# Optimization experiments

Measured on AMD Instinct MI355X. Metric: run time of the kernel, lower is better.

Reference implementation:

```python
import jax, jax.numpy as jnp
import numpy as np
import math

B, I, O, C = 8192, 1024, 1024, 6


def setup_inputs() -> dict:
    key = jax.random.key(0)
    k1, k2, k3, k4 = jax.random.split(key, 4)
    inputs = jax.random.normal(k1, (B, I), dtype=jnp.float32)
    phase_radians = jax.random.uniform(k2, (B,), dtype=jnp.float32) * (2.0 * math.pi)
    # xavier-uniform per control point: bound = sqrt(6/(I+O))
    bound = math.sqrt(6.0 / (I + O))
    weight_control_points = jax.random.uniform(k3, (C, O, I), dtype=jnp.float32, minval=-bound, maxval=bound)
    bias_control_points = jnp.zeros((C, O), dtype=jnp.float32) + 0.01 * jax.random.normal(k4, (C, O), dtype=jnp.float32)
    return {"inputs": inputs, "phase_radians": phase_radians,
            "weight_control_points": weight_control_points,
            "bias_control_points": bias_control_points}


def _catmull_rom(phase_radians, num_control_points):
    two_pi = 2.0 * math.pi
    phase = jnp.remainder(phase_radians, two_pi)
    position = phase * (float(num_control_points) / two_pi)
    base = jnp.floor(position)
    base_idx = base.astype(jnp.int32)
    t = position - base
    t2 = t * t
    t3 = t2 * t
    indices = jnp.stack([
        jnp.remainder(base_idx - 1, num_control_points),
        jnp.remainder(base_idx, num_control_points),
        jnp.remainder(base_idx + 1, num_control_points),
        jnp.remainder(base_idx + 2, num_control_points),
    ], axis=1)  # [B, 4]
    weights = jnp.stack([
        -0.5 * t + t2 - 0.5 * t3,
        1.0 - 2.5 * t2 + 1.5 * t3,
        0.5 * t + 2.0 * t2 - 1.5 * t3,
        -0.5 * t2 + 0.5 * t3,
    ], axis=1)  # [B, 4]
    return indices, weights


def reference(inputs, phase_radians, weight_control_points, bias_control_points):
    # Faithful to: out[b] = sum_k w[b,k] * (W[idx[b,k]] @ x[b] + bias[idx[b,k]])
    # Instead of materializing [B,O,I] interpolated weights, compute all C
    # control-point projections once and gather the 4 needed per sample.
    num_cp = weight_control_points.shape[0]
    indices, cr_weights = _catmull_rom(phase_radians.astype(inputs.dtype), num_cp)
    y_all = jnp.einsum('coi,bi->bco', weight_control_points, inputs)  # [B, C, O]
    y_sel = jnp.take_along_axis(y_all, indices[:, :, None], axis=1)  # [B, 4, O]
    b_sel = bias_control_points[indices]                              # [B, 4, O]
    return jnp.einsum('bk,bko->bo', cr_weights, y_sel + b_sel)
```

## Files before the change

kernel.cpp:

```cpp
#include <hip/hip_runtime.h>
#include <hip/hip_bf16.h>
#include <math.h>

#define B_SZ 8192
#define I_SZ 1024
#define O_SZ 1024
#define NCP  6

typedef __attribute__((ext_vector_type(8))) short bf16x8;
typedef __attribute__((ext_vector_type(4))) float f32x4;

__device__ __forceinline__ unsigned short f2bf(float f) {
  union { float f; unsigned int u; } v; v.f = f;
  unsigned int u = v.u;
  u += 0x7FFFu + ((u >> 16) & 1u);
  return (unsigned short)(u >> 16);
}

__device__ __forceinline__ int seg_of(float ph) {
  const float two_pi = 6.2831855f;
  const float scale = (float)(6.0 / 6.283185307179586);
  float pm = fmodf(ph, two_pi);
  int bi = (int)floorf(pm * scale);
  return ((bi % NCP) + NCP) % NCP;
}

__global__ __launch_bounds__(1024) void prep_all(
    const float* __restrict__ x, unsigned short* __restrict__ xb,
    const float* __restrict__ w, unsigned short* __restrict__ wb,
    const float* __restrict__ phase,
    unsigned short* __restrict__ perm,
    int* __restrict__ blkinfo) {
  __shared__ int scanbuf[1024][NCP];
  __shared__ int ownh[1024][NCP];
  __shared__ int cum[NCP + 1];
  int t = (int)threadIdx.x;
  int b = (int)blockIdx.x;

  if (b < 1024) {
    const int n4 = B_SZ * I_SZ / 4;
    int idx = b * 1024 + t;
    for (int i = idx; i < n4; i += 1024 * 1024) {
      float4 v = reinterpret_cast<const float4*>(x)[i];
      ushort4 o;
      o.x = f2bf(v.x); o.y = f2bf(v.y); o.z = f2bf(v.z); o.w = f2bf(v.w);
      reinterpret_cast<ushort4*>(xb)[i] = o;
    }
    return;
  }
  if (b < 2048) {
    const int n4 = NCP * O_SZ * I_SZ / 4;
    int idx = (b - 1024) * 1024 + t;
    for (int i = idx; i < n4; i += 1024 * 1024) {
      float4 v = reinterpret_cast<const float4*>(w)[i];
      ushort4 o;
      o.x = f2bf(v.x); o.y = f2bf(v.y); o.z = f2bf(v.z); o.w = f2bf(v.w);
      reinterpret_cast<ushort4*>(wb)[i] = o;
    }
    return;
  }

  int segs[8];
#pragma unroll
  for (int s = 0; s < NCP; ++s) scanbuf[t][s] = 0;
#pragma unroll
  for (int i = 0; i < 8; ++i) {
    segs[i] = seg_of(phase[t * 8 + i]);
    scanbuf[t][segs[i]]++;
  }
#pragma unroll
  for (int s = 0; s < NCP; ++s) ownh[t][s] = scanbuf[t][s];
  __syncthreads();
  for (int d = 1; d < 1024; d <<= 1) {
    int add[NCP];
    if (t >= d) {
#pragma unroll
      for (int s = 0; s < NCP; ++s) add[s] = scanbuf[t - d][s];
    }
    __syncthreads();
    if (t >= d) {
#pragma unroll
      for (int s = 0; s < NCP; ++s) scanbuf[t][s] += add[s];
    }
    __syncthreads();
  }
  if (t == 0) {
    cum[0] = 0;
    for (int s = 0; s < NCP; ++s) cum[s + 1] = cum[s] + scanbuf[1023][s];
  }
  __syncthreads();
#pragma unroll
  for (int s = 0; s < NCP; ++s)
    ownh[t][s] = cum[s] + scanbuf[t][s] - ownh[t][s];
#pragma unroll
  for (int i = 0; i < 8; ++i) {
    int s = segs[i];
    perm[ownh[t][s]++] = (unsigned short)(t * 8 + i);
  }
  if (t < B_SZ / 256) {
    int start = t * 256, end = start + 255;
    int s0 = 0; while (s0 < NCP - 1 && cum[s0 + 1] <= start) ++s0;
    int s1 = 0; while (s1 < NCP - 1 && cum[s1 + 1] <= end) ++s1;
    int nj = s1 - s0 + 4; if (nj > NCP) nj = NCP;
    blkinfo[2 * t] = (s0 + NCP - 1) % NCP;
    blkinfo[2 * t + 1] = nj;
  }
}

__device__ __forceinline__ void gload_lds16(const void* g, void* l) {
  __builtin_amdgcn_global_load_lds(
      (const __attribute__((address_space(1))) void*)g,
      (__attribute__((address_space(3))) void*)l, 16, 0, 0);
}

#define BM 256
#define BN 128
#define BK 64
#define NBUF 3

__global__ __launch_bounds__(512, 1) void pfl_gemm(
    const unsigned short* __restrict__ xb,
    const unsigned short* __restrict__ wb,
    const float* __restrict__ phase,
    const unsigned short* __restrict__ perm,
    const int* __restrict__ blkinfo,
    const float* __restrict__ bias,
    float* __restrict__ out) {
  __shared__ __align__(16) unsigned short Abuf[NBUF][BM * BK];
  __shared__ __align__(16) unsigned short Bbuf[NBUF][BN * BK];
  __shared__ __align__(16) float c4[NCP][BM];
  __shared__ int pblk[BM];

  const int nbn = O_SZ / BN;
  int bid = (int)blockIdx.x;
  int swz = (bid & 7) * 32 + (bid >> 3);
  int rowblk = swz / nbn;
  int brow = rowblk * BM;
  int bcol = (swz % nbn) * BN;

  int tid = (int)threadIdx.x;
  int lane = tid & 63;
  int wid = tid >> 6;
  int wr = wid >> 1;
  int wc = wid & 1;

  int jlo = blkinfo[2 * rowblk];
  int NTb = blkinfo[2 * rowblk + 1] << 4;

  if (tid < BM) {
    int orow = (int)perm[brow + tid];
    pblk[tid] = orow;
    float ph = phase[orow];
    const float two_pi = 6.2831855f;
    float pm = fmodf(ph, two_pi);
    float pos = pm * (float)(6.0 / 6.283185307179586);
    float base = floorf(pos);
    int bi = (int)base;
    float t = pos - base;
    float t2 = t * t, t3 = t2 * t;
    float w0 = -0.5f * t + t2 - 0.5f * t3;
    float w1 = 1.0f - 2.5f * t2 + 1.5f * t3;
    float w2 = 0.5f * t + 2.0f * t2 - 1.5f * t3;
    float w3 = -0.5f * t2 + 0.5f * t3;
    float cc[NCP] = {0.f, 0.f, 0.f, 0.f, 0.f, 0.f};
    cc[((bi - 1) % NCP + NCP) % NCP] += w0;
    cc[(bi % NCP + NCP) % NCP]       += w1;
    cc[((bi + 1) % NCP + NCP) % NCP] += w2;
    cc[((bi + 2) % NCP + NCP) % NCP] += w3;
    for (int j = 0; j < NCP; ++j) c4[j][tid] = cc[j];
  }

  f32x4 acc[4][4];
  f32x4 part[4][4];
#pragma unroll
  for (int m = 0; m < 4; ++m)
#pragma unroll
    for (int n = 0; n < 4; ++n) {
      acc[m][n] = (f32x4){0.f, 0.f, 0.f, 0.f};
      part[m][n] = (f32x4){0.f, 0.f, 0.f, 0.f};
    }

  int swzcol = ((lane & 7) ^ (lane >> 3)) * 8;
  int r0 = brow + wid * 8 + (lane >> 3);
  const unsigned short* xsP0 = xb + (size_t)perm[r0      ] * I_SZ + swzcol;
  const unsigned short* xsP1 = xb + (size_t)perm[r0 +  64] * I_SZ + swzcol;
  const unsigned short* xsP2 = xb + (size_t)perm[r0 + 128] * I_SZ + swzcol;
  const unsigned short* xsP3 = xb + (size_t)perm[r0 + 192] * I_SZ + swzcol;
  const unsigned short* wsrc =
      wb + (size_t)(bcol + wid * 8 + (lane >> 3)) * I_SZ + swzcol;

  int lbase = (lane & 15) * 128 + (((lane >> 4) ^ (lane & 7)) & 7) * 16;

  auto STAGE = [&](int t, int b) {
    int ks = (t & 15) * 64;
    int cN = jlo + (t >> 4); if (cN >= NCP) cN -= NCP;
    const unsigned short* ws = wsrc + (size_t)cN * O_SZ * I_SZ + ks;
    unsigned short* Ad = &Abuf[b][(wid * 8) * BK];
    unsigned short* Bd = &Bbuf[b][(wid * 8) * BK];
    gload_lds16(xsP0 + ks, Ad);
    gload_lds16(xsP1 + ks, Ad + 64 * BK);
    gload_lds16(xsP2 + ks, Ad + 128 * BK);
    gload_lds16(xsP3 + ks, Ad + 192 * BK);
    gload_lds16(ws, Bd);
    gload_lds16(ws + (size_t)64 * I_SZ, Bd + 64 * BK);
  };

  STAGE(0, 0);
  STAGE(1, 1);
  asm volatile("s_waitcnt vmcnt(6)" ::: "memory");
  __builtin_amdgcn_sched_barrier(0);
  __syncthreads();

  int cur = 0;
  for (int t = 0; t < NTb; ++t) {
    const char* Ab = (const char*)&Abuf[cur][0];
    const char* Bb = (const char*)&Bbuf[cur][0];
    int st = cur + 2; if (st >= NBUF) st -= NBUF;

    bf16x8 af0[4], bf0[4], af1[4], bf1[4];
#pragma unroll
    for (int m = 0; m < 4; ++m)
      af0[m] = *reinterpret_cast<const bf16x8*>(
          Ab + (wr * 64 + m * 16) * 128 + lbase);
#pragma unroll
    for (int n = 0; n < 4; ++n)
      bf0[n] = *reinterpret_cast<const bf16x8*>(
          Bb + (wc * 64 + n * 16) * 128 + lbase);
    if (t + 2 < NTb) STAGE(t + 2, st);
    asm volatile("s_waitcnt lgkmcnt(0)" ::: "memory");
    __builtin_amdgcn_sched_barrier(0);

#pragma unroll
    for (int m = 0; m < 4; ++m)
      af1[m] = *reinterpret_cast<const bf16x8*>(
          Ab + (wr * 64 + m * 16) * 128 + (lbase ^ 64));
#pragma unroll
    for (int n = 0; n < 4; ++n)
      bf1[n] = *reinterpret_cast<const bf16x8*>(
          Bb + (wc * 64 + n * 16) * 128 + (lbase ^ 64));
    __builtin_amdgcn_sched_barrier(0);

    __builtin_amdgcn_s_setprio(1);
#pragma unroll
    for (int m = 0; m < 4; ++m)
#pragma unroll
      for (int n = 0; n < 4; ++n)
        part[m][n] = __builtin_amdgcn_mfma_f32_16x16x32_bf16(
            af0[m], bf0[n], part[m][n], 0, 0, 0);
    __builtin_amdgcn_s_setprio(0);

    asm volatile("s_waitcnt lgkmcnt(0)" ::: "memory");
    __builtin_amdgcn_sched_barrier(0);

    __builtin_amdgcn_s_setprio(1);
#pragma unroll
    for (int m = 0; m < 4; ++m)
#pragma unroll
      for (int n = 0; n < 4; ++n)
        part[m][n] = __builtin_amdgcn_mfma_f32_16x16x32_bf16(
            af1[m], bf1[n], part[m][n], 0, 0, 0);
    __builtin_amdgcn_s_setprio(0);

    if ((t & 15) == 15) {
      int cj = jlo + (t >> 4); if (cj >= NCP) cj -= NCP;
#pragma unroll
      for (int m = 0; m < 4; ++m) {
        f32x4 cv = *reinterpret_cast<const f32x4*>(
            &c4[cj][wr * 64 + m * 16 + (lane >> 4) * 4]);
#pragma unroll
        for (int n = 0; n < 4; ++n) {
          acc[m][n] += cv * part[m][n];
          part[m][n] = (f32x4){0.f, 0.f, 0.f, 0.f};
        }
      }
    }

    if (t + 2 < NTb)
      asm volatile("s_waitcnt vmcnt(6)" ::: "memory");
    else
      asm volatile("s_waitcnt vmcnt(0)" ::: "memory");
    __builtin_amdgcn_sched_barrier(0);
    __builtin_amdgcn_s_barrier();
    ++cur; if (cur == NBUF) cur = 0;
  }

#pragma unroll
  for (int n = 0; n < 4; ++n) {
    int col = bcol + wc * 64 + n * 16 + (lane & 15);
    float b6[NCP];
#pragma unroll
    for (int j = 0; j < NCP; ++j) b6[j] = bias[j * O_SZ + col];
#pragma unroll
    for (int m = 0; m < 4; ++m) {
#pragma unroll
      for (int r = 0; r < 4; ++r) {
        int rloc = wr * 64 + m * 16 + (lane >> 4) * 4 + r;
        float s = 0.f;
#pragma unroll
        for (int j = 0; j < NCP; ++j) s += c4[j][rloc] * b6[j];
        out[(size_t)pblk[rloc] * O_SZ + col] = acc[m][n][r] + s;
      }
    }
  }
}

extern "C" void kernel_launch(void* const* d_in, const int* in_sizes, int n_in,
                              void* d_out, int out_size, void* d_ws, size_t ws_size,
                              hipStream_t stream) {
  (void)in_sizes; (void)n_in; (void)out_size; (void)ws_size;
  const float* x     = (const float*)d_in[0];
  const float* phase = (const float*)d_in[1];
  const float* w     = (const float*)d_in[2];
  const float* bias  = (const float*)d_in[3];
  float* out = (float*)d_out;

  char* ws = (char*)d_ws;
  unsigned short* xb = (unsigned short*)ws;
  unsigned short* wb = (unsigned short*)(ws + (size_t)16 * 1024 * 1024);
  unsigned short* perm = (unsigned short*)(ws + (size_t)28 * 1024 * 1024);
  int* blkinfo = (int*)(ws + (size_t)28 * 1024 * 1024 + 16384);

  prep_all<<<2049, 1024, 0, stream>>>(x, xb, w, wb, phase, perm, blkinfo);

  dim3 grid((B_SZ / BM) * (O_SZ / BN));
  pfl_gemm<<<grid, 512, 0, stream>>>(xb, wb, phase, perm, blkinfo, bias, out);
}
```

Before: 110.8 us.

## Software-pipeline LDS fragment loads across barrier to overlap with MFMA

Restructures the main K loop so the first-half A/B fragments for the next tile are read from LDS right after the barrier, while the second-half MFMAs of the current tile are still pending. The first-half MFMAs now issue while the second-half LDS reads are still in flight (lgkmcnt(8)). The goal is to hide LDS read latency behind matrix work instead of stalling on lgkmcnt(0) before each MFMA block. In exchange it keeps two full fragment sets live in registers and makes the barrier and waitcnt ordering more delicate.

```diff
diff --git a/kernel.cpp b/kernel.cpp
--- a/kernel.cpp
+++ b/kernel.cpp
@@ -211,77 +211,94 @@
   __builtin_amdgcn_sched_barrier(0);
   __syncthreads();
 
+  bf16x8 afA[4], bfA[4], afB[4], bfB[4];
+  {
+    const char* Ab = (const char*)&Abuf[0][0];
+    const char* Bb = (const char*)&Bbuf[0][0];
+#pragma unroll
+    for (int m = 0; m < 4; ++m)
+      afA[m] = *reinterpret_cast<const bf16x8*>(
+          Ab + (wr * 64 + m * 16) * 128 + lbase);
+#pragma unroll
+    for (int n = 0; n < 4; ++n)
+      bfA[n] = *reinterpret_cast<const bf16x8*>(
+          Bb + (wc * 64 + n * 16) * 128 + lbase);
+  }
+
   int cur = 0;
   for (int t = 0; t < NTb; ++t) {
     const char* Ab = (const char*)&Abuf[cur][0];
     const char* Bb = (const char*)&Bbuf[cur][0];
     int st = cur + 2; if (st >= NBUF) st -= NBUF;
-
-    bf16x8 af0[4], bf0[4], af1[4], bf1[4];
+    int nxt = cur + 1; if (nxt >= NBUF) nxt -= NBUF;
+
 #pragma unroll
     for (int m = 0; m < 4; ++m)
-      af0[m] = *reinterpret_cast<const bf16x8*>(
-          Ab + (wr * 64 + m * 16) * 128 + lbase);
+      afB[m] = *reinterpret_cast<const bf16x8*>(
+          Ab + (wr * 64 + m * 16) * 128 + (lbase ^ 64));
 #pragma unroll
     for (int n = 0; n < 4; ++n)
-      bf0[n] = *reinterpret_cast<const bf16x8*>(
-          Bb + (wc * 64 + n * 16) * 128 + lbase);
+      bfB[n] = *reinterpret_cast<const bf16x8*>(
+          Bb + (wc * 64 + n * 16) * 128 + (lbase ^ 64));
     if (t + 2 < NTb) STAGE(t + 2, st);
+    asm volatile("s_waitcnt lgkmcnt(8)" ::: "memory");
+    __builtin_amdgcn_sched_barrier(0);
+
+    __builtin_amdgcn_s_setprio(1);
+#pragma unroll
+    for (int m = 0; m < 4; ++m)
+#pragma unroll
+      for (int n = 0; n < 4; ++n)
+        part[m][n] = __builtin_amdgcn_mfma_f32_16x16x32_bf16(
+            afA[m], bfA[n], part[m][n], 0, 0, 0);
+    __builtin_amdgcn_s_setprio(0);
+
     asm volatile("s_waitcnt lgkmcnt(0)" ::: "memory");
     __builtin_amdgcn_sched_barrier(0);
-
-#pragma unroll
-    for (int m = 0; m < 4; ++m)
-      af1[m] = *reinterpret_cast<const bf16x8*>(
-          Ab + (wr * 64 + m * 16) * 128 + (lbase ^ 64));
-#pragma unroll
-    for (int n = 0; n < 4; ++n)
-      bf1[n] = *reinterpret_cast<const bf16x8*>(
-          Bb + (wc * 64 + n * 16) * 128 + (lbase ^ 64));
-    __builtin_amdgcn_sched_barrier(0);
-
-    __builtin_amdgcn_s_setprio(1);
-#pragma unroll
-    for (int m = 0; m < 4; ++m)
-#pragma unroll
-      for (int n = 0; n < 4; ++n)
-        part[m][n] = __builtin_amdgcn_mfma_f32_16x16x32_bf16(
-            af0[m], bf0[n], part[m][n], 0, 0, 0);
-    __builtin_amdgcn_s_setprio(0);
-
-    asm volatile("s_waitcnt lgkmcnt(0)" ::: "memory");
-    __builtin_amdgcn_sched_barrier(0);
-
-    __builtin_amdgcn_s_setprio(1);
-#pragma unroll
-    for (int m = 0; m < 4; ++m)
-#pragma unroll
-      for (int n = 0; n < 4; ++n)
-        part[m][n] = __builtin_amdgcn_mfma_f32_16x16x32_bf16(
-            af1[m], bf1[n], part[m][n], 0, 0, 0);
-    __builtin_amdgcn_s_setprio(0);
-
-    if ((t & 15) == 15) {
-      int cj = jlo + (t >> 4); if (cj >= NCP) cj -= NCP;
-#pragma unroll
-      for (int m = 0; m < 4; ++m) {
-        f32x4 cv = *reinterpret_cast<const f32x4*>(
-            &c4[cj][wr * 64 + m * 16 + (lane >> 4) * 4]);
-#pragma unroll
-        for (int n = 0; n < 4; ++n) {
-          acc[m][n] += cv * part[m][n];
-          part[m][n] = (f32x4){0.f, 0.f, 0.f, 0.f};
-        }
-      }
-    }
-
     if (t + 2 < NTb)
       asm volatile("s_waitcnt vmcnt(6)" ::: "memory");
     else
       asm volatile("s_waitcnt vmcnt(0)" ::: "memory");
     __builtin_amdgcn_sched_barrier(0);
     __builtin_amdgcn_s_barrier();
-    ++cur; if (cur == NBUF) cur = 0;
+
+    if (t + 1 < NTb) {
+      const char* Ab2 = (const char*)&Abuf[nxt][0];
+      const char* Bb2 = (const char*)&Bbuf[nxt][0];
+#pragma unroll
+      for (int m = 0; m < 4; ++m)
+        afA[m] = *reinterpret_cast<const bf16x8*>(
+            Ab2 + (wr * 64 + m * 16) * 128 + lbase);
+#pragma unroll
+      for (int n = 0; n < 4; ++n)
+        bfA[n] = *reinterpret_cast<const bf16x8*>(
+            Bb2 + (wc * 64 + n * 16) * 128 + lbase);
+    }
+    __builtin_amdgcn_sched_barrier(0);
+
+    __builtin_amdgcn_s_setprio(1);
+#pragma unroll
+    for (int m = 0; m < 4; ++m)
+#pragma unroll
+      for (int n = 0; n < 4; ++n)
+        part[m][n] = __builtin_amdgcn_mfma_f32_16x16x32_bf16(
+            afB[m], bfB[n], part[m][n], 0, 0, 0);
+    __builtin_amdgcn_s_setprio(0);
+
+    if ((t & 15) == 15) {
+      int cj = jlo + (t >> 4); if (cj >= NCP) cj -= NCP;
+#pragma unroll
+      for (int m = 0; m < 4; ++m) {
+        f32x4 cv = *reinterpret_cast<const f32x4*>(
+            &c4[cj][wr * 64 + m * 16 + (lane >> 4) * 4]);
+#pragma unroll
+        for (int n = 0; n < 4; ++n) {
+          acc[m][n] += cv * part[m][n];
+          part[m][n] = (f32x4){0.f, 0.f, 0.f, 0.f};
+        }
+      }
+    }
+    cur = nxt;
   }
 
 #pragma unroll
```

Measured after the change: 103.7 us. -6.4%, faster.
